# Kernel optimization log

Hardware: AMD Instinct MI355X
Metric: run time of the kernel (lower is better)

## Reference

```python
import jax, jax.numpy as jnp
import numpy as np

NEG_INF = -1e9  # additive mask value (every row attends to itself, so softmax is safe)


def setup_inputs() -> dict:
    D, H, N = 256, 8, 4096
    key = jax.random.key(0)
    ks = jax.random.split(key, 7)
    slots = jax.random.normal(ks[0], (1, N, D), dtype=jnp.float32)
    batch_idx = jnp.sort(jax.random.randint(ks[1], (N,), 0, 16)).astype(jnp.int32)
    s_in = 1.0 / np.sqrt(D)
    w_in = jax.random.uniform(ks[2], (3 * D, D), jnp.float32, -s_in, s_in)
    b_in = jnp.zeros((3 * D,), jnp.float32)
    w_out = jax.random.uniform(ks[3], (D, D), jnp.float32, -s_in, s_in)
    b_out = jnp.zeros((D,), jnp.float32)
    ln_gamma = jnp.ones((D,), jnp.float32)
    ln_beta = jnp.zeros((D,), jnp.float32)
    return {"slots": slots, "batch_idx": batch_idx, "w_in": w_in, "b_in": b_in,
            "w_out": w_out, "b_out": b_out, "ln_gamma": ln_gamma, "ln_beta": ln_beta}


def _mha_block_diag(x, batch_idx, w_in, b_in, w_out, b_out, num_heads):
    # x: [N, D]
    N, D = x.shape
    hd = D // num_heads
    qkv = x @ w_in.T + b_in                      # [N, 3D]
    q, k, v = jnp.split(qkv, 3, axis=-1)
    q = q.reshape(N, num_heads, hd).transpose(1, 0, 2)   # [H, N, hd]
    k = k.reshape(N, num_heads, hd).transpose(1, 0, 2)
    v = v.reshape(N, num_heads, hd).transpose(1, 0, 2)
    scale = 1.0 / np.sqrt(hd)
    scores = jnp.einsum('hnd,hmd->hnm', q, k) * scale    # [H, N, N]
    mask = batch_idx[:, None] != batch_idx[None, :]      # True = blocked
    scores = jnp.where(mask[None], NEG_INF, scores)
    attn = jax.nn.softmax(scores, axis=-1)
    out = jnp.einsum('hnm,hmd->hnd', attn, v)            # [H, N, hd]
    out = out.transpose(1, 0, 2).reshape(N, D)
    return out @ w_out.T + b_out


def _layer_norm(x, gamma, beta, eps=1e-5):
    mu = jnp.mean(x, axis=-1, keepdims=True)
    var = jnp.mean(jnp.square(x - mu), axis=-1, keepdims=True)
    return (x - mu) * jax.lax.rsqrt(var + eps) * gamma + beta


def reference(slots, batch_idx, w_in, b_in, w_out, b_out, ln_gamma, ln_beta):
    # slots: [1, N, D]; dropout prob is 0.0 (eval-mode reference)
    x = slots[0]
    delta = _mha_block_diag(x, batch_idx, w_in, b_in, w_out, b_out, num_heads=8)
    out = _layer_norm(x + delta, ln_gamma, ln_beta)
    return out[None]
```

## Files before the change

kernel.cpp:

```cpp
#include <hip/hip_runtime.h>
#include <hip/hip_bf16.h>

#define NROWS 4096
#define DMODEL 256
#define NHEADS 8
#define HD 32

typedef __attribute__((ext_vector_type(8))) short short8;
typedef __attribute__((ext_vector_type(4))) float f32x4;

__global__ __launch_bounds__(256) void prep_kernel(
    const float* __restrict__ slots, const float* __restrict__ w_in,
    const float* __restrict__ w_out, const int* __restrict__ bidx,
    __hip_bfloat16* __restrict__ Abf, __hip_bfloat16* __restrict__ Winb,
    __hip_bfloat16* __restrict__ Woutb, int* __restrict__ segs) {
  const int bid = blockIdx.x;
  const float* src;
  __hip_bfloat16* dst;
  int i;
  if (bid < 1024)      { src = slots; dst = Abf;   i = (bid * 256 + (int)threadIdx.x) * 4; }
  else if (bid < 1216) { src = w_in;  dst = Winb;  i = ((bid - 1024) * 256 + (int)threadIdx.x) * 4; }
  else if (bid < 1280) { src = w_out; dst = Woutb; i = ((bid - 1216) * 256 + (int)threadIdx.x) * 4; }
  else {
    const int r = (bid - 1280) * 256 + threadIdx.x;
    const int b = bidx[r];
    if (r == 0 || bidx[r - 1] != b) segs[b] = r;
    if (r == NROWS - 1 || bidx[r + 1] != b) segs[16 + b] = r + 1;
    return;
  }
  const float4 v = *(const float4*)(src + i);
  __hip_bfloat162 lo, hi;
  lo.x = __float2bfloat16(v.x); lo.y = __float2bfloat16(v.y);
  hi.x = __float2bfloat16(v.z); hi.y = __float2bfloat16(v.w);
  *(__hip_bfloat162*)(dst + i) = lo;
  *(__hip_bfloat162*)(dst + i + 2) = hi;
}

__global__ __launch_bounds__(256, 4) void gemm_qkv(
    const __hip_bfloat16* __restrict__ A,
    const __hip_bfloat16* __restrict__ B,
    const float* __restrict__ bias,
    __hip_bfloat16* __restrict__ Qo,
    __hip_bfloat16* __restrict__ Ko,
    __hip_bfloat16* __restrict__ Vo) {
  const int wv   = threadIdx.x >> 6;
  const int lane = threadIdx.x & 63;
  const int lo16 = lane & 15;
  const int quad = lane >> 4;
  const int bm = blockIdx.y * 64 + wv * 16;
  const int bn = blockIdx.x * 64;

  f32x4 acc[4] = {};
  #pragma unroll
  for (int k0 = 0; k0 < 256; k0 += 32) {
    const short8 af = *(const short8*)(A + (size_t)(bm + lo16) * 256 + k0 + quad * 8);
    #pragma unroll
    for (int ni = 0; ni < 4; ni++) {
      const short8 bf = *(const short8*)(B + (size_t)(bn + ni * 16 + lo16) * 256 + k0 + quad * 8);
      acc[ni] = __builtin_amdgcn_mfma_f32_16x16x32_bf16(af, bf, acc[ni], 0, 0, 0);
    }
  }
  #pragma unroll
  for (int ni = 0; ni < 4; ni++) {
    const int col = bn + ni * 16 + lo16;
    const int sel = col >> 8;
    const int h = (col & 255) >> 5;
    const int d = col & 31;
    const float bv = bias[col];
    #pragma unroll
    for (int r = 0; r < 4; r++) {
      const int n = bm + quad * 4 + r;
      const __hip_bfloat16 v = __float2bfloat16(acc[ni][r] + bv);
      if (sel == 0)      Qo[((size_t)h * NROWS + n) * HD + d] = v;
      else if (sel == 1) Ko[((size_t)h * NROWS + n) * HD + d] = v;
      else               Vo[((size_t)h * HD + d) * NROWS + n] = v;
    }
  }
}

__global__ __launch_bounds__(256, 4) void attn_mfma(
    const __hip_bfloat16* __restrict__ Qb,
    const __hip_bfloat16* __restrict__ Kb,
    const __hip_bfloat16* __restrict__ Vt,
    const int* __restrict__ bidx,
    const int* __restrict__ segs,
    __hip_bfloat16* __restrict__ out)
{
  __shared__ __align__(16) __hip_bfloat16 Plds_all[4][16][40];
  __shared__ __align__(16) float alds_all[4][16];
  __shared__ float mld[4][16], lld[4][16];
  __shared__ float Old[4][16][32];
  const int wv   = threadIdx.x >> 6;
  const int lane = threadIdx.x & 63;
  const int qt   = blockIdx.x >> 3;
  const int h    = blockIdx.x & 7;
  const int r0   = qt * 16;
  const int lo16 = lane & 15;
  const int quad = lane >> 4;
  __hip_bfloat16 (*Plds)[40] = Plds_all[wv];
  float* alds = alds_all[wv];

  const int bq  = bidx[r0 + lo16];
  const int stq = segs[bq];
  const unsigned rng = (unsigned)(segs[16 + bq] - stq);

  const int kstart = segs[bidx[r0]] & ~31;
  const int kend   = segs[16 + bidx[r0 + 15]];
  const int ntiles = (kend - kstart + 31) >> 5;

  const short8 qf = *(const short8*)(Qb + ((size_t)h * NROWS + r0 + lo16) * HD + quad * 8);

  f32x4 o0 = {0.f, 0.f, 0.f, 0.f}, o1 = {0.f, 0.f, 0.f, 0.f};
  float m = -1e30f, l = 0.0f;
  const float scale2 = 0.17677669529663687f * 1.4426950408889634f;

  for (int t = wv; t < ntiles; t += 4) {
    const int c0 = kstart + t * 32;
    const short8 kf0 = *(const short8*)(Kb + ((size_t)h * NROWS + c0 + lo16) * HD + quad * 8);
    const short8 kf1 = *(const short8*)(Kb + ((size_t)h * NROWS + c0 + 16 + lo16) * HD + quad * 8);
    const int vc = c0 + quad * 8;
    const short8 vf0 = *(const short8*)(Vt + ((size_t)h * HD + lo16) * NROWS + vc);
    const short8 vf1 = *(const short8*)(Vt + ((size_t)h * HD + 16 + lo16) * NROWS + vc);

    const f32x4 z = {0.f, 0.f, 0.f, 0.f};
    f32x4 s0 = __builtin_amdgcn_mfma_f32_16x16x32_bf16(kf0, qf, z, 0, 0, 0);
    f32x4 s1 = __builtin_amdgcn_mfma_f32_16x16x32_bf16(kf1, qf, z, 0, 0, 0);

    const int kb = c0 + quad * 4 - stq;
    float p0v[4], p1v[4];
    float mx = -3e38f;
    #pragma unroll
    for (int r = 0; r < 4; r++) {
      const float sc0 = ((unsigned)(kb + r)      < rng) ? s0[r] * scale2 : -3e38f;
      const float sc1 = ((unsigned)(kb + 16 + r) < rng) ? s1[r] * scale2 : -3e38f;
      p0v[r] = sc0; p1v[r] = sc1;
      mx = fmaxf(mx, fmaxf(sc0, sc1));
    }
    mx = fmaxf(mx, __shfl_xor(mx, 16));
    mx = fmaxf(mx, __shfl_xor(mx, 32));
    const float nm = fmaxf(m, mx);
    float ps = 0.0f;
    #pragma unroll
    for (int r = 0; r < 4; r++) {
      p0v[r] = __builtin_amdgcn_exp2f(p0v[r] - nm);
      p1v[r] = __builtin_amdgcn_exp2f(p1v[r] - nm);
      ps += p0v[r] + p1v[r];
    }
    ps += __shfl_xor(ps, 16);
    ps += __shfl_xor(ps, 32);

    const float alpha = __builtin_amdgcn_exp2f(m - nm);
    l = l * alpha + ps;
    if (!__all(nm == m)) {
      if (quad == 0) alds[lo16] = alpha;
      const f32x4 av = *(const f32x4*)&alds[quad * 4];
      #pragma unroll
      for (int r = 0; r < 4; r++) { o0[r] *= av[r]; o1[r] *= av[r]; }
    }
    m = nm;

    {
      __hip_bfloat162* pw0 = (__hip_bfloat162*)&Plds[lo16][quad * 4];
      __hip_bfloat162* pw1 = (__hip_bfloat162*)&Plds[lo16][16 + quad * 4];
      __hip_bfloat162 a, b;
      a.x = __float2bfloat16(p0v[0]); a.y = __float2bfloat16(p0v[1]);
      b.x = __float2bfloat16(p0v[2]); b.y = __float2bfloat16(p0v[3]);
      pw0[0] = a; pw0[1] = b;
      a.x = __float2bfloat16(p1v[0]); a.y = __float2bfloat16(p1v[1]);
      b.x = __float2bfloat16(p1v[2]); b.y = __float2bfloat16(p1v[3]);
      pw1[0] = a; pw1[1] = b;
    }
    const short8 pf = *(const short8*)&Plds[lo16][quad * 8];
    o0 = __builtin_amdgcn_mfma_f32_16x16x32_bf16(pf, vf0, o0, 0, 0, 0);
    o1 = __builtin_amdgcn_mfma_f32_16x16x32_bf16(pf, vf1, o1, 0, 0, 0);
  }

  #pragma unroll
  for (int r = 0; r < 4; r++) {
    const int row = quad * 4 + r;
    Old[wv][row][lo16]      = o0[r];
    Old[wv][row][lo16 + 16] = o1[r];
  }
  if (quad == 0) { mld[wv][lo16] = m; lld[wv][lo16] = l; }
  __syncthreads();

  const int row = threadIdx.x >> 4;
  const int c   = threadIdx.x & 15;
  float M = fmaxf(fmaxf(mld[0][row], mld[1][row]),
                  fmaxf(mld[2][row], mld[3][row]));
  float L = 0.f, O0 = 0.f, O1 = 0.f;
  #pragma unroll
  for (int w = 0; w < 4; w++) {
    const float e = __builtin_amdgcn_exp2f(mld[w][row] - M);
    L  += e * lld[w][row];
    O0 += e * Old[w][row][c];
    O1 += e * Old[w][row][c + 16];
  }
  const float inv = 1.0f / L;
  const int grow = r0 + row;
  out[(size_t)grow * DMODEL + h * HD + c]      = __float2bfloat16(O0 * inv);
  out[(size_t)grow * DMODEL + h * HD + 16 + c] = __float2bfloat16(O1 * inv);
}

__global__ __launch_bounds__(256, 4) void gemm_out_ln(
    const __hip_bfloat16* __restrict__ A,
    const __hip_bfloat16* __restrict__ B,
    const float* __restrict__ bias,
    const float* __restrict__ x,
    const float* __restrict__ gamma, const float* __restrict__ beta,
    float* __restrict__ out) {
  __shared__ float red1[16][4], red2[16][4];
  const int wv   = threadIdx.x >> 6;
  const int lane = threadIdx.x & 63;
  const int lo16 = lane & 15;
  const int quad = lane >> 4;
  const int r0 = blockIdx.x * 16;
  const int wn = wv * 64;

  f32x4 acc[4] = {};
  #pragma unroll
  for (int k0 = 0; k0 < 256; k0 += 32) {
    const short8 af = *(const short8*)(A + (size_t)(r0 + lo16) * 256 + k0 + quad * 8);
    #pragma unroll
    for (int ni = 0; ni < 4; ni++) {
      const short8 bf = *(const short8*)(B + (size_t)(wn + ni * 16 + lo16) * 256 + k0 + quad * 8);
      acc[ni] = __builtin_amdgcn_mfma_f32_16x16x32_bf16(af, bf, acc[ni], 0, 0, 0);
    }
  }

  float val[4][4];
  float s1[4] = {}, s2[4] = {};
  #pragma unroll
  for (int ni = 0; ni < 4; ni++) {
    const int col = wn + ni * 16 + lo16;
    const float bv = bias[col];
    #pragma unroll
    for (int r = 0; r < 4; r++) {
      const int row = r0 + quad * 4 + r;
      const float v = acc[ni][r] + bv + x[(size_t)row * DMODEL + col];
      val[ni][r] = v;
      s1[r] += v;
      s2[r] += v * v;
    }
  }
  #pragma unroll
  for (int r = 0; r < 4; r++) {
    #pragma unroll
    for (int off = 1; off < 16; off <<= 1) {
      s1[r] += __shfl_xor(s1[r], off);
      s2[r] += __shfl_xor(s2[r], off);
    }
    if (lo16 == 0) { red1[quad * 4 + r][wv] = s1[r]; red2[quad * 4 + r][wv] = s2[r]; }
  }
  __syncthreads();
  #pragma unroll
  for (int r = 0; r < 4; r++) {
    const int lrow = quad * 4 + r;
    const float mean = (red1[lrow][0] + red1[lrow][1] + red1[lrow][2] + red1[lrow][3]) * (1.0f / DMODEL);
    const float ex2  = (red2[lrow][0] + red2[lrow][1] + red2[lrow][2] + red2[lrow][3]) * (1.0f / DMODEL);
    const float rstd = rsqrtf(fmaxf(ex2 - mean * mean, 0.0f) + 1e-5f);
    const int row = r0 + lrow;
    #pragma unroll
    for (int ni = 0; ni < 4; ni++) {
      const int col = wn + ni * 16 + lo16;
      out[(size_t)row * DMODEL + col] =
          (val[ni][r] - mean) * rstd * gamma[col] + beta[col];
    }
  }
}

extern "C" void kernel_launch(void* const* d_in, const int* in_sizes, int n_in,
                              void* d_out, int out_size, void* d_ws, size_t ws_size,
                              hipStream_t stream) {
  const float* slots  = (const float*)d_in[0];
  const int*   bidx   = (const int*)  d_in[1];
  const float* w_in   = (const float*)d_in[2];
  const float* b_in   = (const float*)d_in[3];
  const float* w_out  = (const float*)d_in[4];
  const float* b_out  = (const float*)d_in[5];
  const float* ln_g   = (const float*)d_in[6];
  const float* ln_b   = (const float*)d_in[7];
  float* out = (float*)d_out;

  char* ws = (char*)d_ws;
  __hip_bfloat16* Abf   = (__hip_bfloat16*)(ws);
  __hip_bfloat16* Qb    = (__hip_bfloat16*)(ws + (2u  << 20));
  __hip_bfloat16* Kb    = (__hip_bfloat16*)(ws + (4u  << 20));
  __hip_bfloat16* Vt    = (__hip_bfloat16*)(ws + (6u  << 20));
  __hip_bfloat16* attnb = (__hip_bfloat16*)(ws + (8u  << 20));
  __hip_bfloat16* Winb  = (__hip_bfloat16*)(ws + (10u << 20));
  __hip_bfloat16* Woutb = (__hip_bfloat16*)(ws + (10u << 20) + (512u << 10));
  int*            segs  = (int*)           (ws + (11u << 20));

  prep_kernel<<<1296, 256, 0, stream>>>(slots, w_in, w_out, bidx,
                                        Abf, Winb, Woutb, segs);
  {
    dim3 grid(768 / 64, NROWS / 64);
    gemm_qkv<<<grid, 256, 0, stream>>>(Abf, Winb, b_in, Qb, Kb, Vt);
  }
  attn_mfma<<<(NROWS / 16) * NHEADS, 256, 0, stream>>>(Qb, Kb, Vt, bidx,
                                                       segs, attnb);
  gemm_out_ln<<<NROWS / 16, 256, 0, stream>>>(attnb, Woutb, b_out, slots,
                                              ln_g, ln_b, out);
}
```

Measured before the change: 113.0 us.

## Fuse bf16 conversion into QKV GEMM and fuse attention with output projection+LayerNorm

Removes the separate fp32-to-bf16 prep kernel by converting inputs and weights on the fly inside the QKV GEMM, which also computes the segment table. Attention now uses one block per 16-row tile with 8 waves (one per head), each wave running all key tiles serially with register prefetch of the next K/V tile, replacing the cross-wave split-softmax merge. The per-head outputs are staged in shared memory and fed directly into the output projection and LayerNorm in the same kernel. This cuts two launches and the intermediate attention-output buffer round trip, at the cost of less key-dimension parallelism per head and repeated fp32 weight conversion in every block.

```diff
diff --git a/kernel.cpp b/kernel.cpp
--- a/kernel.cpp
+++ b/kernel.cpp
@@ -9,54 +9,49 @@
 typedef __attribute__((ext_vector_type(8))) short short8;
 typedef __attribute__((ext_vector_type(4))) float f32x4;
 
-__global__ __launch_bounds__(256) void prep_kernel(
-    const float* __restrict__ slots, const float* __restrict__ w_in,
-    const float* __restrict__ w_out, const int* __restrict__ bidx,
-    __hip_bfloat16* __restrict__ Abf, __hip_bfloat16* __restrict__ Winb,
-    __hip_bfloat16* __restrict__ Woutb, int* __restrict__ segs) {
+__device__ __forceinline__ short bf16raw(float x) {
+  return (short)__builtin_bit_cast(unsigned short, __float2bfloat16(x));
+}
+__device__ __forceinline__ short8 cvt8(const float4 a, const float4 b) {
+  short8 r;
+  r[0] = bf16raw(a.x); r[1] = bf16raw(a.y); r[2] = bf16raw(a.z); r[3] = bf16raw(a.w);
+  r[4] = bf16raw(b.x); r[5] = bf16raw(b.y); r[6] = bf16raw(b.z); r[7] = bf16raw(b.w);
+  return r;
+}
+
+__global__ __launch_bounds__(256, 4) void gemm_qkv_f32(
+    const float* __restrict__ A,
+    const float* __restrict__ W,
+    const float* __restrict__ bias,
+    const int* __restrict__ bidx,
+    int* __restrict__ segs,
+    __hip_bfloat16* __restrict__ Qo,
+    __hip_bfloat16* __restrict__ Ko,
+    __hip_bfloat16* __restrict__ Vo) {
   const int bid = blockIdx.x;
-  const float* src;
-  __hip_bfloat16* dst;
-  int i;
-  if (bid < 1024)      { src = slots; dst = Abf;   i = (bid * 256 + (int)threadIdx.x) * 4; }
-  else if (bid < 1216) { src = w_in;  dst = Winb;  i = ((bid - 1024) * 256 + (int)threadIdx.x) * 4; }
-  else if (bid < 1280) { src = w_out; dst = Woutb; i = ((bid - 1216) * 256 + (int)threadIdx.x) * 4; }
-  else {
-    const int r = (bid - 1280) * 256 + threadIdx.x;
+  if (bid >= 768) {
+    const int r = (bid - 768) * 256 + threadIdx.x;
     const int b = bidx[r];
     if (r == 0 || bidx[r - 1] != b) segs[b] = r;
     if (r == NROWS - 1 || bidx[r + 1] != b) segs[16 + b] = r + 1;
     return;
   }
-  const float4 v = *(const float4*)(src + i);
-  __hip_bfloat162 lo, hi;
-  lo.x = __float2bfloat16(v.x); lo.y = __float2bfloat16(v.y);
-  hi.x = __float2bfloat16(v.z); hi.y = __float2bfloat16(v.w);
-  *(__hip_bfloat162*)(dst + i) = lo;
-  *(__hip_bfloat162*)(dst + i + 2) = hi;
-}
-
-__global__ __launch_bounds__(256, 4) void gemm_qkv(
-    const __hip_bfloat16* __restrict__ A,
-    const __hip_bfloat16* __restrict__ B,
-    const float* __restrict__ bias,
-    __hip_bfloat16* __restrict__ Qo,
-    __hip_bfloat16* __restrict__ Ko,
-    __hip_bfloat16* __restrict__ Vo) {
   const int wv   = threadIdx.x >> 6;
   const int lane = threadIdx.x & 63;
   const int lo16 = lane & 15;
   const int quad = lane >> 4;
-  const int bm = blockIdx.y * 64 + wv * 16;
-  const int bn = blockIdx.x * 64;
+  const int bm = (bid / 12) * 64 + wv * 16;
+  const int bn = (bid % 12) * 64;
 
   f32x4 acc[4] = {};
   #pragma unroll
   for (int k0 = 0; k0 < 256; k0 += 32) {
-    const short8 af = *(const short8*)(A + (size_t)(bm + lo16) * 256 + k0 + quad * 8);
+    const float* ap = A + (size_t)(bm + lo16) * 256 + k0 + quad * 8;
+    const short8 af = cvt8(*(const float4*)ap, *(const float4*)(ap + 4));
     #pragma unroll
     for (int ni = 0; ni < 4; ni++) {
-      const short8 bf = *(const short8*)(B + (size_t)(bn + ni * 16 + lo16) * 256 + k0 + quad * 8);
+      const float* wp = W + (size_t)(bn + ni * 16 + lo16) * 256 + k0 + quad * 8;
+      const short8 bf = cvt8(*(const float4*)wp, *(const float4*)(wp + 4));
       acc[ni] = __builtin_amdgcn_mfma_f32_16x16x32_bf16(af, bf, acc[ni], 0, 0, 0);
     }
   }
@@ -78,25 +73,29 @@
   }
 }
 
-__global__ __launch_bounds__(256, 4) void attn_mfma(
+__global__ __launch_bounds__(512, 2) void attn_out_ln(
     const __hip_bfloat16* __restrict__ Qb,
     const __hip_bfloat16* __restrict__ Kb,
     const __hip_bfloat16* __restrict__ Vt,
     const int* __restrict__ bidx,
     const int* __restrict__ segs,
-    __hip_bfloat16* __restrict__ out)
+    const float* __restrict__ w_out,
+    const float* __restrict__ bias,
+    const float* __restrict__ x,
+    const float* __restrict__ gamma, const float* __restrict__ beta,
+    float* __restrict__ out)
 {
-  __shared__ __align__(16) __hip_bfloat16 Plds_all[4][16][40];
-  __shared__ __align__(16) float alds_all[4][16];
-  __shared__ float mld[4][16], lld[4][16];
-  __shared__ float Old[4][16][32];
+  __shared__ __align__(16) __hip_bfloat16 Plds_all[8][16][40];
+  __shared__ __align__(16) float alds_all[8][16];
+  __shared__ __align__(16) __hip_bfloat16 att[16][264];
+  __shared__ float red1[16][8], red2[16][8];
+
   const int wv   = threadIdx.x >> 6;
   const int lane = threadIdx.x & 63;
-  const int qt   = blockIdx.x >> 3;
-  const int h    = blockIdx.x & 7;
-  const int r0   = qt * 16;
   const int lo16 = lane & 15;
   const int quad = lane >> 4;
+  const int r0   = blockIdx.x * 16;
+  const int h    = wv;
   __hip_bfloat16 (*Plds)[40] = Plds_all[wv];
   float* alds = alds_all[wv];
 
@@ -107,6 +106,7 @@
   const int kstart = segs[bidx[r0]] & ~31;
   const int kend   = segs[16 + bidx[r0 + 15]];
   const int ntiles = (kend - kstart + 31) >> 5;
+  const int tlast  = kstart + (ntiles - 1) * 32;
 
   const short8 qf = *(const short8*)(Qb + ((size_t)h * NROWS + r0 + lo16) * HD + quad * 8);
 
@@ -114,13 +114,18 @@
   float m = -1e30f, l = 0.0f;
   const float scale2 = 0.17677669529663687f * 1.4426950408889634f;
 
-  for (int t = wv; t < ntiles; t += 4) {
-    const int c0 = kstart + t * 32;
-    const short8 kf0 = *(const short8*)(Kb + ((size_t)h * NROWS + c0 + lo16) * HD + quad * 8);
-    const short8 kf1 = *(const short8*)(Kb + ((size_t)h * NROWS + c0 + 16 + lo16) * HD + quad * 8);
-    const int vc = c0 + quad * 8;
-    const short8 vf0 = *(const short8*)(Vt + ((size_t)h * HD + lo16) * NROWS + vc);
-    const short8 vf1 = *(const short8*)(Vt + ((size_t)h * HD + 16 + lo16) * NROWS + vc);
+  int c0 = kstart;
+  short8 kf0 = *(const short8*)(Kb + ((size_t)h * NROWS + c0 + lo16) * HD + quad * 8);
+  short8 kf1 = *(const short8*)(Kb + ((size_t)h * NROWS + c0 + 16 + lo16) * HD + quad * 8);
+  short8 vf0 = *(const short8*)(Vt + ((size_t)h * HD + lo16) * NROWS + c0 + quad * 8);
+  short8 vf1 = *(const short8*)(Vt + ((size_t)h * HD + 16 + lo16) * NROWS + c0 + quad * 8);
+
+  for (int t = 0; t < ntiles; t++) {
+    const int c0n = min(c0 + 32, tlast);
+    const short8 nk0 = *(const short8*)(Kb + ((size_t)h * NROWS + c0n + lo16) * HD + quad * 8);
+    const short8 nk1 = *(const short8*)(Kb + ((size_t)h * NROWS + c0n + 16 + lo16) * HD + quad * 8);
+    const short8 nv0 = *(const short8*)(Vt + ((size_t)h * HD + lo16) * NROWS + c0n + quad * 8);
+    const short8 nv1 = *(const short8*)(Vt + ((size_t)h * HD + 16 + lo16) * NROWS + c0n + quad * 8);
 
     const f32x4 z = {0.f, 0.f, 0.f, 0.f};
     f32x4 s0 = __builtin_amdgcn_mfma_f32_16x16x32_bf16(kf0, qf, z, 0, 0, 0);
@@ -173,65 +178,39 @@
     const short8 pf = *(const short8*)&Plds[lo16][quad * 8];
     o0 = __builtin_amdgcn_mfma_f32_16x16x32_bf16(pf, vf0, o0, 0, 0, 0);
     o1 = __builtin_amdgcn_mfma_f32_16x16x32_bf16(pf, vf1, o1, 0, 0, 0);
-  }
-
-  #pragma unroll
-  for (int r = 0; r < 4; r++) {
-    const int row = quad * 4 + r;
-    Old[wv][row][lo16]      = o0[r];
-    Old[wv][row][lo16 + 16] = o1[r];
-  }
-  if (quad == 0) { mld[wv][lo16] = m; lld[wv][lo16] = l; }
+
+    c0 = c0n; kf0 = nk0; kf1 = nk1; vf0 = nv0; vf1 = nv1;
+  }
+
+  if (quad == 0) alds[lo16] = 1.0f / l;
+  {
+    const f32x4 inv4 = *(const f32x4*)&alds[quad * 4];
+    #pragma unroll
+    for (int r = 0; r < 4; r++) {
+      const int row = quad * 4 + r;
+      att[row][h * HD + lo16]      = __float2bfloat16(o0[r] * inv4[r]);
+      att[row][h * HD + 16 + lo16] = __float2bfloat16(o1[r] * inv4[r]);
+    }
+  }
   __syncthreads();
 
-  const int row = threadIdx.x >> 4;
-  const int c   = threadIdx.x & 15;
-  float M = fmaxf(fmaxf(mld[0][row], mld[1][row]),
-                  fmaxf(mld[2][row], mld[3][row]));
-  float L = 0.f, O0 = 0.f, O1 = 0.f;
-  #pragma unroll
-  for (int w = 0; w < 4; w++) {
-    const float e = __builtin_amdgcn_exp2f(mld[w][row] - M);
-    L  += e * lld[w][row];
-    O0 += e * Old[w][row][c];
-    O1 += e * Old[w][row][c + 16];
-  }
-  const float inv = 1.0f / L;
-  const int grow = r0 + row;
-  out[(size_t)grow * DMODEL + h * HD + c]      = __float2bfloat16(O0 * inv);
-  out[(size_t)grow * DMODEL + h * HD + 16 + c] = __float2bfloat16(O1 * inv);
-}
-
-__global__ __launch_bounds__(256, 4) void gemm_out_ln(
-    const __hip_bfloat16* __restrict__ A,
-    const __hip_bfloat16* __restrict__ B,
-    const float* __restrict__ bias,
-    const float* __restrict__ x,
-    const float* __restrict__ gamma, const float* __restrict__ beta,
-    float* __restrict__ out) {
-  __shared__ float red1[16][4], red2[16][4];
-  const int wv   = threadIdx.x >> 6;
-  const int lane = threadIdx.x & 63;
-  const int lo16 = lane & 15;
-  const int quad = lane >> 4;
-  const int r0 = blockIdx.x * 16;
-  const int wn = wv * 64;
-
-  f32x4 acc[4] = {};
+  const int wn = wv * 32;
+  f32x4 acc[2] = {};
   #pragma unroll
   for (int k0 = 0; k0 < 256; k0 += 32) {
-    const short8 af = *(const short8*)(A + (size_t)(r0 + lo16) * 256 + k0 + quad * 8);
-    #pragma unroll
-    for (int ni = 0; ni < 4; ni++) {
-      const short8 bf = *(const short8*)(B + (size_t)(wn + ni * 16 + lo16) * 256 + k0 + quad * 8);
+    const short8 af = *(const short8*)&att[lo16][k0 + quad * 8];
+    #pragma unroll
+    for (int ni = 0; ni < 2; ni++) {
+      const float* wp = w_out + (size_t)(wn + ni * 16 + lo16) * 256 + k0 + quad * 8;
+      const short8 bf = cvt8(*(const float4*)wp, *(const float4*)(wp + 4));
       acc[ni] = __builtin_amdgcn_mfma_f32_16x16x32_bf16(af, bf, acc[ni], 0, 0, 0);
     }
   }
 
-  float val[4][4];
+  float val[2][4];
   float s1[4] = {}, s2[4] = {};
   #pragma unroll
-  for (int ni = 0; ni < 4; ni++) {
+  for (int ni = 0; ni < 2; ni++) {
     const int col = wn + ni * 16 + lo16;
     const float bv = bias[col];
     #pragma unroll
@@ -256,12 +235,18 @@
   #pragma unroll
   for (int r = 0; r < 4; r++) {
     const int lrow = quad * 4 + r;
-    const float mean = (red1[lrow][0] + red1[lrow][1] + red1[lrow][2] + red1[lrow][3]) * (1.0f / DMODEL);
-    const float ex2  = (red2[lrow][0] + red2[lrow][1] + red2[lrow][2] + red2[lrow][3]) * (1.0f / DMODEL);
+    const f32x4 ra = *(const f32x4*)&red1[lrow][0];
+    const f32x4 rb = *(const f32x4*)&red1[lrow][4];
+    const f32x4 qa = *(const f32x4*)&red2[lrow][0];
+    const f32x4 qb = *(const f32x4*)&red2[lrow][4];
+    const float t1 = ((ra[0] + ra[1]) + (ra[2] + ra[3])) + ((rb[0] + rb[1]) + (rb[2] + rb[3]));
+    const float t2 = ((qa[0] + qa[1]) + (qa[2] + qa[3])) + ((qb[0] + qb[1]) + (qb[2] + qb[3]));
+    const float mean = t1 * (1.0f / DMODEL);
+    const float ex2  = t2 * (1.0f / DMODEL);
     const float rstd = rsqrtf(fmaxf(ex2 - mean * mean, 0.0f) + 1e-5f);
     const int row = r0 + lrow;
     #pragma unroll
-    for (int ni = 0; ni < 4; ni++) {
+    for (int ni = 0; ni < 2; ni++) {
       const int col = wn + ni * 16 + lo16;
       out[(size_t)row * DMODEL + col] =
           (val[ni][r] - mean) * rstd * gamma[col] + beta[col];
@@ -283,23 +268,14 @@
   float* out = (float*)d_out;
 
   char* ws = (char*)d_ws;
-  __hip_bfloat16* Abf   = (__hip_bfloat16*)(ws);
-  __hip_bfloat16* Qb    = (__hip_bfloat16*)(ws + (2u  << 20));
-  __hip_bfloat16* Kb    = (__hip_bfloat16*)(ws + (4u  << 20));
-  __hip_bfloat16* Vt    = (__hip_bfloat16*)(ws + (6u  << 20));
-  __hip_bfloat16* attnb = (__hip_bfloat16*)(ws + (8u  << 20));
-  __hip_bfloat16* Winb  = (__hip_bfloat16*)(ws + (10u << 20));
-  __hip_bfloat16* Woutb = (__hip_bfloat16*)(ws + (10u << 20) + (512u << 10));
-  int*            segs  = (int*)           (ws + (11u << 20));
-
-  prep_kernel<<<1296, 256, 0, stream>>>(slots, w_in, w_out, bidx,
-                                        Abf, Winb, Woutb, segs);
-  {
-    dim3 grid(768 / 64, NROWS / 64);
-    gemm_qkv<<<grid, 256, 0, stream>>>(Abf, Winb, b_in, Qb, Kb, Vt);
-  }
-  attn_mfma<<<(NROWS / 16) * NHEADS, 256, 0, stream>>>(Qb, Kb, Vt, bidx,
-                                                       segs, attnb);
-  gemm_out_ln<<<NROWS / 16, 256, 0, stream>>>(attnb, Woutb, b_out, slots,
+  __hip_bfloat16* Qb   = (__hip_bfloat16*)(ws);
+  __hip_bfloat16* Kb   = (__hip_bfloat16*)(ws + (2u << 20));
+  __hip_bfloat16* Vt   = (__hip_bfloat16*)(ws + (4u << 20));
+  int*            segs = (int*)           (ws + (6u << 20));
+
+  gemm_qkv_f32<<<784, 256, 0, stream>>>(slots, w_in, b_in, bidx, segs,
+                                        Qb, Kb, Vt);
+  attn_out_ln<<<NROWS / 16, 512, 0, stream>>>(Qb, Kb, Vt, bidx, segs,
+                                              w_out, b_out, slots,
                                               ln_g, ln_b, out);
 }
```

Measured after the change: 123.7 us. +9.5%, slower.

## Widen attention key tile to 64, add MFMA priority, swizzle QKV GEMM blocks

Applied to the files above, without the earlier changes.

The attention kernel now handles 64 keys per wave iteration instead of 32, issuing four QK and four PV MFMAs per tile. The wider tile halves the number of softmax reductions, shuffles and rescale checks per key, and s_setprio raises priority around the MFMA groups. The QKV GEMM moves to a 1D grid with an XCD-style block swizzle to improve L2 locality. Coarser tiles waste more masked work at segment boundaries and raise register pressure.

```diff
diff --git a/kernel.cpp b/kernel.cpp
--- a/kernel.cpp
+++ b/kernel.cpp
@@ -43,12 +43,14 @@
     __hip_bfloat16* __restrict__ Qo,
     __hip_bfloat16* __restrict__ Ko,
     __hip_bfloat16* __restrict__ Vo) {
+  const int bid = blockIdx.x;
+  const int swz = (bid & 7) * 96 + (bid >> 3);
+  const int bn = (swz % 12) * 64;
   const int wv   = threadIdx.x >> 6;
   const int lane = threadIdx.x & 63;
   const int lo16 = lane & 15;
   const int quad = lane >> 4;
-  const int bm = blockIdx.y * 64 + wv * 16;
-  const int bn = blockIdx.x * 64;
+  const int bm = (swz / 12) * 64 + wv * 16;
 
   f32x4 acc[4] = {};
   #pragma unroll
@@ -86,7 +88,7 @@
     const int* __restrict__ segs,
     __hip_bfloat16* __restrict__ out)
 {
-  __shared__ __align__(16) __hip_bfloat16 Plds_all[4][16][40];
+  __shared__ __align__(16) __hip_bfloat16 Plds_all[4][16][72];
   __shared__ __align__(16) float alds_all[4][16];
   __shared__ float mld[4][16], lld[4][16];
   __shared__ float Old[4][16][32];
@@ -97,16 +99,16 @@
   const int r0   = qt * 16;
   const int lo16 = lane & 15;
   const int quad = lane >> 4;
-  __hip_bfloat16 (*Plds)[40] = Plds_all[wv];
+  __hip_bfloat16 (*Plds)[72] = Plds_all[wv];
   float* alds = alds_all[wv];
 
   const int bq  = bidx[r0 + lo16];
   const int stq = segs[bq];
   const unsigned rng = (unsigned)(segs[16 + bq] - stq);
 
-  const int kstart = segs[bidx[r0]] & ~31;
+  const int kstart = segs[bidx[r0]] & ~63;
   const int kend   = segs[16 + bidx[r0 + 15]];
-  const int ntiles = (kend - kstart + 31) >> 5;
+  const int ntiles = (kend - kstart + 63) >> 6;
 
   const short8 qf = *(const short8*)(Qb + ((size_t)h * NROWS + r0 + lo16) * HD + quad * 8);
 
@@ -115,36 +117,50 @@
   const float scale2 = 0.17677669529663687f * 1.4426950408889634f;
 
   for (int t = wv; t < ntiles; t += 4) {
-    const int c0 = kstart + t * 32;
-    const short8 kf0 = *(const short8*)(Kb + ((size_t)h * NROWS + c0 + lo16) * HD + quad * 8);
-    const short8 kf1 = *(const short8*)(Kb + ((size_t)h * NROWS + c0 + 16 + lo16) * HD + quad * 8);
-    const int vc = c0 + quad * 8;
-    const short8 vf0 = *(const short8*)(Vt + ((size_t)h * HD + lo16) * NROWS + vc);
-    const short8 vf1 = *(const short8*)(Vt + ((size_t)h * HD + 16 + lo16) * NROWS + vc);
+    const int c0 = kstart + t * 64;
+    const __hip_bfloat16* kbase = Kb + ((size_t)h * NROWS + c0 + lo16) * HD + quad * 8;
+    const short8 kf0 = *(const short8*)(kbase);
+    const short8 kf1 = *(const short8*)(kbase + 16 * HD);
+    const short8 kf2 = *(const short8*)(kbase + 32 * HD);
+    const short8 kf3 = *(const short8*)(kbase + 48 * HD);
+    const __hip_bfloat16* vbase = Vt + ((size_t)h * HD + lo16) * NROWS + c0 + quad * 8;
+    const short8 vA0 = *(const short8*)(vbase);
+    const short8 vA1 = *(const short8*)(vbase + 32);
+    const short8 vB0 = *(const short8*)(vbase + 16 * NROWS);
+    const short8 vB1 = *(const short8*)(vbase + 16 * NROWS + 32);
 
     const f32x4 z = {0.f, 0.f, 0.f, 0.f};
-    f32x4 s0 = __builtin_amdgcn_mfma_f32_16x16x32_bf16(kf0, qf, z, 0, 0, 0);
-    f32x4 s1 = __builtin_amdgcn_mfma_f32_16x16x32_bf16(kf1, qf, z, 0, 0, 0);
+    __builtin_amdgcn_s_setprio(1);
+    f32x4 sv[4];
+    sv[0] = __builtin_amdgcn_mfma_f32_16x16x32_bf16(kf0, qf, z, 0, 0, 0);
+    sv[1] = __builtin_amdgcn_mfma_f32_16x16x32_bf16(kf1, qf, z, 0, 0, 0);
+    sv[2] = __builtin_amdgcn_mfma_f32_16x16x32_bf16(kf2, qf, z, 0, 0, 0);
+    sv[3] = __builtin_amdgcn_mfma_f32_16x16x32_bf16(kf3, qf, z, 0, 0, 0);
+    __builtin_amdgcn_s_setprio(0);
 
     const int kb = c0 + quad * 4 - stq;
-    float p0v[4], p1v[4];
+    float p[4][4];
     float mx = -3e38f;
     #pragma unroll
-    for (int r = 0; r < 4; r++) {
-      const float sc0 = ((unsigned)(kb + r)      < rng) ? s0[r] * scale2 : -3e38f;
-      const float sc1 = ((unsigned)(kb + 16 + r) < rng) ? s1[r] * scale2 : -3e38f;
-      p0v[r] = sc0; p1v[r] = sc1;
-      mx = fmaxf(mx, fmaxf(sc0, sc1));
+    for (int g = 0; g < 4; g++) {
+      #pragma unroll
+      for (int r = 0; r < 4; r++) {
+        const float sc = ((unsigned)(kb + g * 16 + r) < rng) ? sv[g][r] * scale2 : -3e38f;
+        p[g][r] = sc;
+        mx = fmaxf(mx, sc);
+      }
     }
     mx = fmaxf(mx, __shfl_xor(mx, 16));
     mx = fmaxf(mx, __shfl_xor(mx, 32));
     const float nm = fmaxf(m, mx);
     float ps = 0.0f;
     #pragma unroll
-    for (int r = 0; r < 4; r++) {
-      p0v[r] = __builtin_amdgcn_exp2f(p0v[r] - nm);
-      p1v[r] = __builtin_amdgcn_exp2f(p1v[r] - nm);
-      ps += p0v[r] + p1v[r];
+    for (int g = 0; g < 4; g++) {
+      #pragma unroll
+      for (int r = 0; r < 4; r++) {
+        p[g][r] = __builtin_amdgcn_exp2f(p[g][r] - nm);
+        ps += p[g][r];
+      }
     }
     ps += __shfl_xor(ps, 16);
     ps += __shfl_xor(ps, 32);
@@ -159,20 +175,22 @@
     }
     m = nm;
 
-    {
-      __hip_bfloat162* pw0 = (__hip_bfloat162*)&Plds[lo16][quad * 4];
-      __hip_bfloat162* pw1 = (__hip_bfloat162*)&Plds[lo16][16 + quad * 4];
+    #pragma unroll
+    for (int g = 0; g < 4; g++) {
+      __hip_bfloat162* pw = (__hip_bfloat162*)&Plds[lo16][g * 16 + quad * 4];
       __hip_bfloat162 a, b;
-      a.x = __float2bfloat16(p0v[0]); a.y = __float2bfloat16(p0v[1]);
-      b.x = __float2bfloat16(p0v[2]); b.y = __float2bfloat16(p0v[3]);
-      pw0[0] = a; pw0[1] = b;
-      a.x = __float2bfloat16(p1v[0]); a.y = __float2bfloat16(p1v[1]);
-      b.x = __float2bfloat16(p1v[2]); b.y = __float2bfloat16(p1v[3]);
-      pw1[0] = a; pw1[1] = b;
-    }
-    const short8 pf = *(const short8*)&Plds[lo16][quad * 8];
-    o0 = __builtin_amdgcn_mfma_f32_16x16x32_bf16(pf, vf0, o0, 0, 0, 0);
-    o1 = __builtin_amdgcn_mfma_f32_16x16x32_bf16(pf, vf1, o1, 0, 0, 0);
+      a.x = __float2bfloat16(p[g][0]); a.y = __float2bfloat16(p[g][1]);
+      b.x = __float2bfloat16(p[g][2]); b.y = __float2bfloat16(p[g][3]);
+      pw[0] = a; pw[1] = b;
+    }
+    const short8 pf0 = *(const short8*)&Plds[lo16][quad * 8];
+    const short8 pf1 = *(const short8*)&Plds[lo16][32 + quad * 8];
+    __builtin_amdgcn_s_setprio(1);
+    o0 = __builtin_amdgcn_mfma_f32_16x16x32_bf16(pf0, vA0, o0, 0, 0, 0);
+    o0 = __builtin_amdgcn_mfma_f32_16x16x32_bf16(pf1, vA1, o0, 0, 0, 0);
+    o1 = __builtin_amdgcn_mfma_f32_16x16x32_bf16(pf0, vB0, o1, 0, 0, 0);
+    o1 = __builtin_amdgcn_mfma_f32_16x16x32_bf16(pf1, vB1, o1, 0, 0, 0);
+    __builtin_amdgcn_s_setprio(0);
   }
 
   #pragma unroll
@@ -294,10 +312,7 @@
 
   prep_kernel<<<1296, 256, 0, stream>>>(slots, w_in, w_out, bidx,
                                         Abf, Winb, Woutb, segs);
-  {
-    dim3 grid(768 / 64, NROWS / 64);
-    gemm_qkv<<<grid, 256, 0, stream>>>(Abf, Winb, b_in, Qb, Kb, Vt);
-  }
+  gemm_qkv<<<768, 256, 0, stream>>>(Abf, Winb, b_in, Qb, Kb, Vt);
   attn_mfma<<<(NROWS / 16) * NHEADS, 256, 0, stream>>>(Qb, Kb, Vt, bidx,
                                                        segs, attnb);
   gemm_out_ln<<<NROWS / 16, 256, 0, stream>>>(attnb, Woutb, b_out, slots,
```

Result: no change. 111.3 us (-1.5%).
